# Performance work log

Measured on AMD Instinct MI355X. Metric: run time of the kernel, lower is better.

## Reference

```python
import jax, jax.numpy as jnp
import numpy as np

D_STATE = 512
D_MODEL = 512
BATCH = 8
SEQ = 4096
DT_MIN, DT_MAX = 1e-3, 0.1
LN_EPS = 1e-5


def setup_inputs() -> dict:
    key = jax.random.key(0)
    ks = jax.random.split(key, 4)
    x = jax.random.normal(ks[0], (BATCH, SEQ, D_MODEL), dtype=jnp.float32)
    volatility_scale = jax.random.uniform(ks[1], (BATCH, SEQ, 1), dtype=jnp.float32)
    # parameters (mirroring the torch module's __init__)
    log_lambda_real = jnp.linspace(np.log(DT_MIN), np.log(DT_MAX), D_STATE).astype(jnp.float32)
    log_b = jax.random.uniform(ks[2], (D_STATE, 1), dtype=jnp.float32, minval=-0.5, maxval=0.5)
    c = jax.random.normal(ks[3], (1, D_STATE), dtype=jnp.float32) / np.sqrt(D_STATE)
    log_d = jnp.zeros((1,), jnp.float32)
    ts = np.array([1.0 / 24.0, 1.0, 5.0, 21.0, 63.0], np.float32)
    extra = np.linspace(63.0, 189.0, D_STATE - len(ts), dtype=np.float32)
    log_step = jnp.log(jnp.asarray(np.concatenate([ts, extra])))
    volatility_gate = jnp.ones((D_MODEL,), jnp.float32)
    alpha = jnp.asarray(0.7, jnp.float32)
    ln_weight = jnp.ones((D_STATE,), jnp.float32)
    ln_bias = jnp.zeros((D_STATE,), jnp.float32)
    return dict(x=x, volatility_scale=volatility_scale,
                log_lambda_real=log_lambda_real, log_b=log_b, c=c, log_d=log_d,
                log_step=log_step, volatility_gate=volatility_gate, alpha=alpha,
                ln_weight=ln_weight, ln_bias=ln_bias)


def reference(x, volatility_scale, log_lambda_real, log_b, c, log_d,
              log_step, volatility_gate, alpha, ln_weight, ln_bias):
    lam = -jnp.exp(log_lambda_real)              # [N], negative real poles
    step = jnp.exp(log_step)                     # [N], per-state timescale
    b = jnp.exp(log_b)[:, 0]                     # [N]
    d = jnp.exp(log_d)                           # [1], skip gain
    # bilinear (Tustin) discretization, paired per state
    z = step * lam                               # [N]
    a_disc = (2.0 + z) / (2.0 - z)               # [N]
    b_disc = step * (1.0 + a_disc) * b / 2.0     # [N]
    gate = jax.nn.sigmoid(volatility_gate)       # [D]
    c_vec = c[0]                                 # [N]

    def layer_norm(h):
        mu = jnp.mean(h, axis=-1, keepdims=True)
        var = jnp.var(h, axis=-1, keepdims=True)
        return (h - mu) * jax.lax.rsqrt(var + LN_EPS) * ln_weight + ln_bias

    def scan_step(h, inp):
        x_t, v_t = inp                           # [B,D], [B,1]
        h = a_disc * h + b_disc * x_t            # diagonal SSM update, [B,N]
        h = layer_norm(h)
        h = h / (1.0 + gate * v_t)               # volatility gating
        y_t = jnp.sum(h * c_vec, axis=-1, keepdims=True) + d * x_t  # [B,D]
        return h, y_t

    h0 = jnp.zeros((x.shape[0], a_disc.shape[0]), x.dtype)
    xs = (jnp.swapaxes(x, 0, 1), jnp.swapaxes(volatility_scale, 0, 1))  # time-major
    _, ys = jax.lax.scan(scan_step, h0, xs)      # [S,B,D]
    y = jnp.swapaxes(ys, 0, 1)                   # [B,S,D]
    al = jax.nn.sigmoid(alpha)
    return al * x + (1.0 - al) * y
```

## Files before the change

### kernel.cpp

```cpp
#include <hip/hip_runtime.h>
#include <cstdint>
#include <cstddef>

#define BATCH 8
#define SEQ   4096
#define DS    512
#define JPL   8
#define BLK   8
#define NBLK  (SEQ / BLK)
#define LN_EPS 1e-5f

typedef float v2f __attribute__((ext_vector_type(2)));
typedef float v4f __attribute__((ext_vector_type(4)));

static __device__ __forceinline__ v2f lo2(v4f x) { return __builtin_shufflevector(x, x, 0, 1); }
static __device__ __forceinline__ v2f hi2(v4f x) { return __builtin_shufflevector(x, x, 2, 3); }

template <int CTRL>
__device__ __forceinline__ float dpp_add(float v) {
  int t = __builtin_amdgcn_update_dpp(0, __builtin_bit_cast(int, v), CTRL, 0xF, 0xF, true);
  return v + __builtin_bit_cast(float, t);
}
__device__ __forceinline__ float wave_sum64(float v) {
  v = dpp_add<0x111>(v);
  v = dpp_add<0x112>(v);
  v = dpp_add<0x114>(v);
  v = dpp_add<0x118>(v);
  v = dpp_add<0x142>(v);
  v = dpp_add<0x143>(v);
  return v;
}
__device__ __forceinline__ float bcast63(float v) {
  return __builtin_bit_cast(float, __builtin_amdgcn_readlane(__builtin_bit_cast(int, v), 63));
}

__device__ __forceinline__ void ld16(const float* g, float* l) {
  __builtin_amdgcn_global_load_lds(
      (const __attribute__((address_space(1))) void*)g,
      (__attribute__((address_space(3))) void*)l, 16, 0, 0);
}

__global__ __launch_bounds__(192, 1) void ssm_scan(
    const float* __restrict__ x, const float* __restrict__ vol,
    const float* __restrict__ llr, const float* __restrict__ logb,
    const float* __restrict__ cvec, const float* __restrict__ lstp,
    const float* __restrict__ vgat, const float* __restrict__ lnw,
    const float* __restrict__ lnb, const float* __restrict__ alph,
    const float* __restrict__ logd, float* __restrict__ out)
{
  __shared__ __attribute__((aligned(16))) float X0[4096], X1[4096];
  __shared__ __attribute__((aligned(16))) float R0[4096], R1[4096];
  __shared__ __attribute__((aligned(16))) float SC0[512], SC1[512];
  __shared__ __attribute__((aligned(16))) float SB0[512], SB1[512];

  const int b    = blockIdx.x;
  const int lane = threadIdx.x & 63;
  const int wid  = threadIdx.x >> 6;

  if (wid == 1) {
    const float* xg = x + (size_t)b * SEQ * DS + lane * JPL;
    float* ob = out + (size_t)b * SEQ * DS;
    float al   = 1.0f / (1.0f + expf(-alph[0]));
    float dd   = expf(logd[0]);
    float coef = __builtin_fmaf(1.0f - al, dd, al);
    float c1   = 1.0f - al;

    auto dma_blk = [&](int blk, float* Xs) {
#pragma unroll
      for (int u = 0; u < BLK; ++u) {
        const float* row = xg + (size_t)(blk * BLK + u) * DS;
        ld16(row,     Xs + u * 512);
        ld16(row + 4, Xs + u * 512 + 256);
      }
    };
    auto out_blk = [&](const float* SCs, const float* Xs, int blk) {
#pragma unroll
      for (int u = 0; u < BLK; ++u) {
        float s  = bcast63(wave_sum64(SCs[u * 64 + lane]));
        float sc = c1 * s;
        v4f xa = *(const v4f*)(Xs + u * 512 + lane * 4);
        v4f xb = *(const v4f*)(Xs + u * 512 + 256 + lane * 4);
        v4f ya = xa * coef + sc;
        v4f yb = xb * coef + sc;
        float* row = ob + (size_t)(blk * BLK + u) * DS + lane * 8;
        *(v4f*)(row)     = ya;
        *(v4f*)(row + 4) = yb;
      }
    };

    dma_blk(0, X0);
    __syncthreads();
#pragma unroll 1
    for (int i2 = 0; i2 < NBLK; i2 += 2) {
      if (i2 > 0) {
        out_blk(SC1, X1, i2 - 1);
        asm volatile("s_waitcnt lgkmcnt(0)" ::: "memory");
        __builtin_amdgcn_sched_barrier(0);
      }
      dma_blk(i2 + 1, X1);
      __syncthreads();
      out_blk(SC0, X0, i2);
      if (i2 + 2 < NBLK) {
        asm volatile("s_waitcnt lgkmcnt(0)" ::: "memory");
        __builtin_amdgcn_sched_barrier(0);
        dma_blk(i2 + 2, X0);
      }
      __syncthreads();
    }
    out_blk(SC1, X1, NBLK - 1);
  } else if (wid == 2) {
    v2f gate[4];
#pragma unroll
    for (int j = 0; j < JPL; ++j)
      gate[j >> 1][j & 1] = 1.0f / (1.0f + expf(-vgat[lane * JPL + j]));
    v4f cb0, cb1;
#pragma unroll
    for (int m = 0; m < 4; ++m) {
      int n0 = lane * JPL + m, n1 = lane * JPL + 4 + m;
      cb0[m] = cvec[n0] * lnb[n0];
      cb1[m] = cvec[n1] * lnb[n1];
    }
    const float* vg = vol + (size_t)b * SEQ;

    auto rg_blk = [&](v4f Va, v4f Vb, float* Rs, float* SBs) {
#pragma unroll
      for (int u = 0; u < BLK; ++u) {
        float vt = (u < 4) ? Va[u] : Vb[u - 4];
        v4f r0, r1;
#pragma unroll
        for (int k = 0; k < 4; ++k) {
          v2f den = gate[k] * vt + 1.0f;
          float q0 = __builtin_amdgcn_rcpf(den.x);
          float q1 = __builtin_amdgcn_rcpf(den.y);
          if (k < 2) { r0[2 * k] = q0; r0[2 * k + 1] = q1; }
          else       { r1[2 * (k - 2)] = q0; r1[2 * (k - 2) + 1] = q1; }
        }
        *(v4f*)(Rs + u * 512 + lane * 4)       = r0;
        *(v4f*)(Rs + u * 512 + 256 + lane * 4) = r1;
        v4f md = cb0 * r0;
        md = __builtin_elementwise_fma(cb1, r1, md);
        v2f mh = lo2(md) + hi2(md);
        SBs[u * 64 + lane] = mh.x + mh.y;
      }
    };

    v4f V0a = *(const v4f*)(vg + 0), V0b = *(const v4f*)(vg + 4);
    v4f V1a = *(const v4f*)(vg + 8), V1b = *(const v4f*)(vg + 12);
    rg_blk(V0a, V0b, R0, SB0);
    __syncthreads();
#pragma unroll 1
    for (int i2 = 0; i2 < NBLK; i2 += 2) {
      if (i2 + 2 < NBLK) {
        V0a = *(const v4f*)(vg + (i2 + 2) * BLK);
        V0b = *(const v4f*)(vg + (i2 + 2) * BLK + 4);
      }
      rg_blk(V1a, V1b, R1, SB1);
      __syncthreads();
      if (i2 + 3 < NBLK) {
        V1a = *(const v4f*)(vg + (i2 + 3) * BLK);
        V1b = *(const v4f*)(vg + (i2 + 3) * BLK + 4);
      }
      if (i2 + 2 < NBLK) rg_blk(V0a, V0b, R0, SB0);
      __syncthreads();
    }
  } else {
    v2f bd[4], aw[4], ab[4], cw[4];
#pragma unroll
    for (int j = 0; j < JPL; ++j) {
      int n = lane * JPL + j;
      float lam = -expf(llr[n]);
      float st  = expf(lstp[n]);
      float z   = st * lam;
      float ad  = (2.0f + z) / (2.0f - z);
      float bdv = st * (1.0f + ad) * expf(logb[n]) * 0.5f;
      float wv  = lnw[n], bi = lnb[n], cv = cvec[n];
      bd[j >> 1][j & 1] = bdv;
      aw[j >> 1][j & 1] = ad * wv;
      ab[j >> 1][j & 1] = ad * bi;
      cw[j >> 1][j & 1] = cv * wv;
    }
    v2f hp[4];
#pragma unroll
    for (int k = 0; k < 4; ++k) hp[k] = (v2f){0.0f, 0.0f};

    auto proc_blk = [&](const float* Xs, const float* Rs, const float* SBs, float* SCs) {
#pragma unroll
      for (int u = 0; u < BLK; ++u) {
        v4f xx0 = *(const v4f*)(Xs + u * 512 + lane * 4);
        v4f xx1 = *(const v4f*)(Xs + u * 512 + 256 + lane * 4);
        v4f rr0 = *(const v4f*)(Rs + u * 512 + lane * 4);
        v4f rr1 = *(const v4f*)(Rs + u * 512 + 256 + lane * 4);
        float u3s = SBs[u * 64 + lane];
        v2f xs[4] = {lo2(xx0), hi2(xx0), lo2(xx1), hi2(xx1)};
        v2f rs[4] = {lo2(rr0), hi2(rr0), lo2(rr1), hi2(rr1)};

        v2f hr[4], q[4], abrs[4];
#pragma unroll
        for (int k = 0; k < 4; ++k) {
          hr[k]   = __builtin_elementwise_fma(bd[k], xs[k], hp[k]);
          q[k]    = rs[k] * hr[k];
          abrs[k] = ab[k] * rs[k];
        }
        v2f t01 = hr[0] + hr[1], t23 = hr[2] + hr[3];
        v2f tt  = t01 + t23;
        float s1 = tt.x + tt.y;
        v2f m01 = hr[0] * hr[0];
        m01 = __builtin_elementwise_fma(hr[1], hr[1], m01);
        v2f m23 = hr[2] * hr[2];
        m23 = __builtin_elementwise_fma(hr[3], hr[3], m23);
        v2f mm = m01 + m23;
        float s2 = mm.x + mm.y;

        s1 = bcast63(wave_sum64(s1));
        s2 = bcast63(wave_sum64(s2));
        float mu  = s1 * (1.0f / DS);
        float m2e = __builtin_fmaf(s2, 1.0f / DS, LN_EPS);
        float var = __builtin_fmaf(-mu, mu, m2e);
        float inv = __builtin_amdgcn_rsqf(var);

        v2f muv = {mu, mu}, invv = {inv, inv};
        v2f tv[4];
#pragma unroll
        for (int k = 0; k < 4; ++k)
          tv[k] = __builtin_elementwise_fma(-muv, rs[k], q[k]);
#pragma unroll
        for (int k = 0; k < 4; ++k) {
          v2f sv = aw[k] * tv[k];
          hp[k]  = __builtin_elementwise_fma(invv, sv, abrs[k]);
        }
        v2f u0 = cw[0] * tv[0];
        u0 = __builtin_elementwise_fma(cw[1], tv[1], u0);
        v2f u2 = cw[2] * tv[2];
        u2 = __builtin_elementwise_fma(cw[3], tv[3], u2);
        v2f uu = u0 + u2;
        float u1s = uu.x + uu.y;
        SCs[u * 64 + lane] = __builtin_fmaf(inv, u1s, u3s);
      }
    };

    __syncthreads();
#pragma unroll 1
    for (int i2 = 0; i2 < NBLK; i2 += 2) {
      proc_blk(X0, R0, SB0, SC0);
      __syncthreads();
      proc_blk(X1, R1, SB1, SC1);
      __syncthreads();
    }
  }
}

extern "C" void kernel_launch(void* const* d_in, const int* in_sizes, int n_in,
                              void* d_out, int out_size, void* d_ws, size_t ws_size,
                              hipStream_t stream) {
  const float* x    = (const float*)d_in[0];
  const float* vol  = (const float*)d_in[1];
  const float* llr  = (const float*)d_in[2];
  const float* logb = (const float*)d_in[3];
  const float* cvec = (const float*)d_in[4];
  const float* logd = (const float*)d_in[5];
  const float* lstp = (const float*)d_in[6];
  const float* vgat = (const float*)d_in[7];
  const float* alph = (const float*)d_in[8];
  const float* lnw  = (const float*)d_in[9];
  const float* lnb  = (const float*)d_in[10];
  float* outf = (float*)d_out;

  ssm_scan<<<BATCH, 192, 0, stream>>>(x, vol, llr, logb, cvec, lstp,
                                      vgat, lnw, lnb, alph, logd, outf);
}
```

Baseline: 676.2 us.

## Deepen x prefetch to four LDS buffers with vmcnt-based barriers

The DMA wave now keeps x blocks in a four-slot LDS ring and prefetches two blocks ahead, using explicit vmcnt waits instead of full __syncthreads. All three waves switch to raw s_barrier with lgkmcnt waits, so the barrier no longer drains outstanding global loads. The goal is to hide global-load latency behind the serial scan wave. The cost is more LDS and fragile hand-counted vmcnt thresholds, which could introduce races if the counts are wrong.

```diff
diff --git a/kernel.cpp b/kernel.cpp
--- a/kernel.cpp
+++ b/kernel.cpp
@@ -15,6 +15,9 @@
 
 static __device__ __forceinline__ v2f lo2(v4f x) { return __builtin_shufflevector(x, x, 0, 1); }
 static __device__ __forceinline__ v2f hi2(v4f x) { return __builtin_shufflevector(x, x, 2, 3); }
+
+#define LGKM0() asm volatile("s_waitcnt lgkmcnt(0)" ::: "memory")
+#define BARRIER() __builtin_amdgcn_s_barrier()
 
 template <int CTRL>
 __device__ __forceinline__ float dpp_add(float v) {
@@ -48,7 +51,7 @@
     const float* __restrict__ lnb, const float* __restrict__ alph,
     const float* __restrict__ logd, float* __restrict__ out)
 {
-  __shared__ __attribute__((aligned(16))) float X0[4096], X1[4096];
+  __shared__ __attribute__((aligned(16))) float X[4][4096];
   __shared__ __attribute__((aligned(16))) float R0[4096], R1[4096];
   __shared__ __attribute__((aligned(16))) float SC0[512], SC1[512];
   __shared__ __attribute__((aligned(16))) float SB0[512], SB1[512];
@@ -88,26 +91,27 @@
       }
     };
 
-    dma_blk(0, X0);
-    __syncthreads();
+    dma_blk(0, X[0]);
+    dma_blk(1, X[1]);
+    asm volatile("s_waitcnt vmcnt(16)" ::: "memory");
+    BARRIER();
+    dma_blk(2, X[2]);
+    asm volatile("s_waitcnt vmcnt(16)" ::: "memory");
+    BARRIER();
 #pragma unroll 1
-    for (int i2 = 0; i2 < NBLK; i2 += 2) {
-      if (i2 > 0) {
-        out_blk(SC1, X1, i2 - 1);
-        asm volatile("s_waitcnt lgkmcnt(0)" ::: "memory");
-        __builtin_amdgcn_sched_barrier(0);
-      }
-      dma_blk(i2 + 1, X1);
-      __syncthreads();
-      out_blk(SC0, X0, i2);
-      if (i2 + 2 < NBLK) {
-        asm volatile("s_waitcnt lgkmcnt(0)" ::: "memory");
-        __builtin_amdgcn_sched_barrier(0);
-        dma_blk(i2 + 2, X0);
-      }
-      __syncthreads();
-    }
-    out_blk(SC1, X1, NBLK - 1);
+    for (int j = 1; j < NBLK; ++j) {
+      out_blk((j & 1) ? SC0 : SC1, X[(j - 1) & 3], j - 1);
+      LGKM0();
+      __builtin_amdgcn_sched_barrier(0);
+      if (j + 2 < NBLK) {
+        dma_blk(j + 2, X[(j + 2) & 3]);
+        asm volatile("s_waitcnt vmcnt(32)" ::: "memory");
+      } else if (j + 1 < NBLK) {
+        asm volatile("s_waitcnt vmcnt(16)" ::: "memory");
+      }
+      BARRIER();
+    }
+    out_blk(SC1, X[(NBLK - 1) & 3], NBLK - 1);
   } else if (wid == 2) {
     v2f gate[4];
 #pragma unroll
@@ -147,7 +151,8 @@
     v4f V0a = *(const v4f*)(vg + 0), V0b = *(const v4f*)(vg + 4);
     v4f V1a = *(const v4f*)(vg + 8), V1b = *(const v4f*)(vg + 12);
     rg_blk(V0a, V0b, R0, SB0);
-    __syncthreads();
+    LGKM0();
+    BARRIER();
 #pragma unroll 1
     for (int i2 = 0; i2 < NBLK; i2 += 2) {
       if (i2 + 2 < NBLK) {
@@ -155,13 +160,15 @@
         V0b = *(const v4f*)(vg + (i2 + 2) * BLK + 4);
       }
       rg_blk(V1a, V1b, R1, SB1);
-      __syncthreads();
+      LGKM0();
+      BARRIER();
       if (i2 + 3 < NBLK) {
         V1a = *(const v4f*)(vg + (i2 + 3) * BLK);
         V1b = *(const v4f*)(vg + (i2 + 3) * BLK + 4);
       }
       if (i2 + 2 < NBLK) rg_blk(V0a, V0b, R0, SB0);
-      __syncthreads();
+      LGKM0();
+      BARRIER();
     }
   } else {
     v2f bd[4], aw[4], ab[4], cw[4];
@@ -238,13 +245,13 @@
       }
     };
 
-    __syncthreads();
+    BARRIER();
 #pragma unroll 1
-    for (int i2 = 0; i2 < NBLK; i2 += 2) {
-      proc_blk(X0, R0, SB0, SC0);
-      __syncthreads();
-      proc_blk(X1, R1, SB1, SC1);
-      __syncthreads();
+    for (int i4 = 0; i4 < NBLK; i4 += 4) {
+      proc_blk(X[0], R0, SB0, SC0); LGKM0(); BARRIER();
+      proc_blk(X[1], R1, SB1, SC1); LGKM0(); BARRIER();
+      proc_blk(X[2], R0, SB0, SC0); LGKM0(); BARRIER();
+      proc_blk(X[3], R1, SB1, SC1); LGKM0(); BARRIER();
     }
   }
 }
```

Result: slower. 741.1 us (+9.6%).

## Collapse warp-specialized pipeline into single wave with register double-buffering

Applied to the files above, without the earlier changes.

Replaces the three-wave producer/consumer design (DMA+output wave, gating wave, scan wave communicating via LDS and __syncthreads) with a single 64-thread wave per batch that loads x and volatility into registers two blocks ahead, computes gating inline, and writes output directly. This removes LDS traffic and block barriers from the serial critical path. In exchange the one wave now does all the gating reciprocals, the extra output reduction, and the global stores on the serial chain. It also relies on register prefetch alone to hide global load latency.

```diff
diff --git a/kernel.cpp b/kernel.cpp
--- a/kernel.cpp
+++ b/kernel.cpp
@@ -6,7 +6,7 @@
 #define SEQ   4096
 #define DS    512
 #define JPL   8
-#define BLK   8
+#define BLK   4
 #define NBLK  (SEQ / BLK)
 #define LN_EPS 1e-5f
 
@@ -34,13 +34,7 @@
   return __builtin_bit_cast(float, __builtin_amdgcn_readlane(__builtin_bit_cast(int, v), 63));
 }
 
-__device__ __forceinline__ void ld16(const float* g, float* l) {
-  __builtin_amdgcn_global_load_lds(
-      (const __attribute__((address_space(1))) void*)g,
-      (__attribute__((address_space(3))) void*)l, 16, 0, 0);
-}
-
-__global__ __launch_bounds__(192, 1) void ssm_scan(
+__global__ __launch_bounds__(64, 1) void ssm_scan(
     const float* __restrict__ x, const float* __restrict__ vol,
     const float* __restrict__ llr, const float* __restrict__ logb,
     const float* __restrict__ cvec, const float* __restrict__ lstp,
@@ -48,204 +42,121 @@
     const float* __restrict__ lnb, const float* __restrict__ alph,
     const float* __restrict__ logd, float* __restrict__ out)
 {
-  __shared__ __attribute__((aligned(16))) float X0[4096], X1[4096];
-  __shared__ __attribute__((aligned(16))) float R0[4096], R1[4096];
-  __shared__ __attribute__((aligned(16))) float SC0[512], SC1[512];
-  __shared__ __attribute__((aligned(16))) float SB0[512], SB1[512];
+  const int b    = blockIdx.x;
+  const int lane = threadIdx.x;
 
-  const int b    = blockIdx.x;
-  const int lane = threadIdx.x & 63;
-  const int wid  = threadIdx.x >> 6;
+  v2f bd[4], aw[4], ab[4], cw[4], cb[4], gate[4];
+#pragma unroll
+  for (int j = 0; j < JPL; ++j) {
+    int n = lane * JPL + j;
+    float lam = -expf(llr[n]);
+    float st  = expf(lstp[n]);
+    float z   = st * lam;
+    float ad  = (2.0f + z) / (2.0f - z);
+    float bdv = st * (1.0f + ad) * expf(logb[n]) * 0.5f;
+    float wv  = lnw[n], bi = lnb[n], cv = cvec[n];
+    bd[j >> 1][j & 1]   = bdv;
+    aw[j >> 1][j & 1]   = ad * wv;
+    ab[j >> 1][j & 1]   = ad * bi;
+    gate[j >> 1][j & 1] = 1.0f / (1.0f + expf(-vgat[n]));
+    cw[j >> 1][j & 1]   = cv * wv;
+    cb[j >> 1][j & 1]   = cv * bi;
+  }
+  float al   = 1.0f / (1.0f + expf(-alph[0]));
+  float dd   = expf(logd[0]);
+  float coef = __builtin_fmaf(1.0f - al, dd, al);
+  float c1   = 1.0f - al;
+#pragma unroll
+  for (int k = 0; k < 4; ++k) { cw[k] = cw[k] * c1; cb[k] = cb[k] * c1; }
 
-  if (wid == 1) {
-    const float* xg = x + (size_t)b * SEQ * DS + lane * JPL;
-    float* ob = out + (size_t)b * SEQ * DS;
-    float al   = 1.0f / (1.0f + expf(-alph[0]));
-    float dd   = expf(logd[0]);
-    float coef = __builtin_fmaf(1.0f - al, dd, al);
-    float c1   = 1.0f - al;
+  const float* xg = x   + (size_t)b * SEQ * DS + lane * JPL;
+  float*       og = out + (size_t)b * SEQ * DS + lane * JPL;
+  const float* vg = vol + (size_t)b * SEQ;
 
-    auto dma_blk = [&](int blk, float* Xs) {
+  v2f hp[4];
 #pragma unroll
-      for (int u = 0; u < BLK; ++u) {
-        const float* row = xg + (size_t)(blk * BLK + u) * DS;
-        ld16(row,     Xs + u * 512);
-        ld16(row + 4, Xs + u * 512 + 256);
+  for (int k = 0; k < 4; ++k) hp[k] = (v2f){0.0f, 0.0f};
+
+  v4f XA[BLK][2], XB[BLK][2];
+  v4f VA, VB;
+
+  auto loadblk = [&](int blk, v4f (&X)[BLK][2], v4f& V) {
+    const float* base = xg + (size_t)blk * BLK * DS;
+#pragma unroll
+    for (int u = 0; u < BLK; ++u) {
+      X[u][0] = *(const v4f*)(base + u * DS);
+      X[u][1] = *(const v4f*)(base + u * DS + 4);
+    }
+    V = *(const v4f*)(vg + blk * BLK);
+  };
+
+  auto procblk = [&](int blk, v4f (&X)[BLK][2], v4f& V) {
+    float* ob = og + (size_t)blk * BLK * DS;
+#pragma unroll
+    for (int u = 0; u < BLK; ++u) {
+      float vt = V[u];
+      v2f rs[4];
+#pragma unroll
+      for (int k = 0; k < 4; ++k) {
+        v2f den = gate[k] * vt + 1.0f;
+        rs[k].x = __builtin_amdgcn_rcpf(den.x);
+        rs[k].y = __builtin_amdgcn_rcpf(den.y);
       }
-    };
-    auto out_blk = [&](const float* SCs, const float* Xs, int blk) {
+      v2f xs[4] = {lo2(X[u][0]), hi2(X[u][0]), lo2(X[u][1]), hi2(X[u][1])};
+
+      v2f hr[4];
 #pragma unroll
-      for (int u = 0; u < BLK; ++u) {
-        float s  = bcast63(wave_sum64(SCs[u * 64 + lane]));
-        float sc = c1 * s;
-        v4f xa = *(const v4f*)(Xs + u * 512 + lane * 4);
-        v4f xb = *(const v4f*)(Xs + u * 512 + 256 + lane * 4);
-        v4f ya = xa * coef + sc;
-        v4f yb = xb * coef + sc;
-        float* row = ob + (size_t)(blk * BLK + u) * DS + lane * 8;
-        *(v4f*)(row)     = ya;
-        *(v4f*)(row + 4) = yb;
+      for (int k = 0; k < 4; ++k)
+        hr[k] = __builtin_elementwise_fma(bd[k], xs[k], hp[k]);
+
+      v2f t01 = hr[0] + hr[1], t23 = hr[2] + hr[3];
+      v2f tt  = t01 + t23;
+      float s1 = tt.x + tt.y;
+      v2f m01 = hr[0] * hr[0];
+      m01 = __builtin_elementwise_fma(hr[1], hr[1], m01);
+      v2f m23 = hr[2] * hr[2];
+      m23 = __builtin_elementwise_fma(hr[3], hr[3], m23);
+      v2f mm = m01 + m23;
+      float s2 = mm.x + mm.y;
+
+      s1 = bcast63(wave_sum64(s1));
+      s2 = bcast63(wave_sum64(s2));
+      float mu  = s1 * (1.0f / DS);
+      float m2e = __builtin_fmaf(s2, 1.0f / DS, LN_EPS);
+      float var = __builtin_fmaf(-mu, mu, m2e);
+      float inv = __builtin_amdgcn_rsqf(var);
+
+      v2f muv = {mu, mu}, invv = {inv, inv};
+      v2f u1 = {0.0f, 0.0f}, u3 = {0.0f, 0.0f};
+#pragma unroll
+      for (int k = 0; k < 4; ++k) {
+        v2f hrm  = hr[k] - muv;
+        v2f tv   = rs[k] * hrm;
+        v2f sv   = aw[k] * tv;
+        v2f abrs = ab[k] * rs[k];
+        hp[k] = __builtin_elementwise_fma(invv, sv, abrs);
+        u1 = __builtin_elementwise_fma(cw[k], tv, u1);
+        u3 = __builtin_elementwise_fma(cb[k], rs[k], u3);
       }
-    };
+      v2f dp = __builtin_elementwise_fma(u1, invv, u3);
+      float dl = dp.x + dp.y;
+      float s = bcast63(wave_sum64(dl));
 
-    dma_blk(0, X0);
-    __syncthreads();
+      v4f o0 = X[u][0] * coef + s;
+      v4f o1 = X[u][1] * coef + s;
+      *(v4f*)(ob + (size_t)u * DS)     = o0;
+      *(v4f*)(ob + (size_t)u * DS + 4) = o1;
+    }
+  };
+
+  loadblk(0, XA, VA);
+  loadblk(1, XB, VB);
 #pragma unroll 1
-    for (int i2 = 0; i2 < NBLK; i2 += 2) {
-      if (i2 > 0) {
-        out_blk(SC1, X1, i2 - 1);
-        asm volatile("s_waitcnt lgkmcnt(0)" ::: "memory");
-        __builtin_amdgcn_sched_barrier(0);
-      }
-      dma_blk(i2 + 1, X1);
-      __syncthreads();
-      out_blk(SC0, X0, i2);
-      if (i2 + 2 < NBLK) {
-        asm volatile("s_waitcnt lgkmcnt(0)" ::: "memory");
-        __builtin_amdgcn_sched_barrier(0);
-        dma_blk(i2 + 2, X0);
-      }
-      __syncthreads();
-    }
-    out_blk(SC1, X1, NBLK - 1);
-  } else if (wid == 2) {
-    v2f gate[4];
-#pragma unroll
-    for (int j = 0; j < JPL; ++j)
-      gate[j >> 1][j & 1] = 1.0f / (1.0f + expf(-vgat[lane * JPL + j]));
-    v4f cb0, cb1;
-#pragma unroll
-    for (int m = 0; m < 4; ++m) {
-      int n0 = lane * JPL + m, n1 = lane * JPL + 4 + m;
-      cb0[m] = cvec[n0] * lnb[n0];
-      cb1[m] = cvec[n1] * lnb[n1];
-    }
-    const float* vg = vol + (size_t)b * SEQ;
-
-    auto rg_blk = [&](v4f Va, v4f Vb, float* Rs, float* SBs) {
-#pragma unroll
-      for (int u = 0; u < BLK; ++u) {
-        float vt = (u < 4) ? Va[u] : Vb[u - 4];
-        v4f r0, r1;
-#pragma unroll
-        for (int k = 0; k < 4; ++k) {
-          v2f den = gate[k] * vt + 1.0f;
-          float q0 = __builtin_amdgcn_rcpf(den.x);
-          float q1 = __builtin_amdgcn_rcpf(den.y);
-          if (k < 2) { r0[2 * k] = q0; r0[2 * k + 1] = q1; }
-          else       { r1[2 * (k - 2)] = q0; r1[2 * (k - 2) + 1] = q1; }
-        }
-        *(v4f*)(Rs + u * 512 + lane * 4)       = r0;
-        *(v4f*)(Rs + u * 512 + 256 + lane * 4) = r1;
-        v4f md = cb0 * r0;
-        md = __builtin_elementwise_fma(cb1, r1, md);
-        v2f mh = lo2(md) + hi2(md);
-        SBs[u * 64 + lane] = mh.x + mh.y;
-      }
-    };
-
-    v4f V0a = *(const v4f*)(vg + 0), V0b = *(const v4f*)(vg + 4);
-    v4f V1a = *(const v4f*)(vg + 8), V1b = *(const v4f*)(vg + 12);
-    rg_blk(V0a, V0b, R0, SB0);
-    __syncthreads();
-#pragma unroll 1
-    for (int i2 = 0; i2 < NBLK; i2 += 2) {
-      if (i2 + 2 < NBLK) {
-        V0a = *(const v4f*)(vg + (i2 + 2) * BLK);
-        V0b = *(const v4f*)(vg + (i2 + 2) * BLK + 4);
-      }
-      rg_blk(V1a, V1b, R1, SB1);
-      __syncthreads();
-      if (i2 + 3 < NBLK) {
-        V1a = *(const v4f*)(vg + (i2 + 3) * BLK);
-        V1b = *(const v4f*)(vg + (i2 + 3) * BLK + 4);
-      }
-      if (i2 + 2 < NBLK) rg_blk(V0a, V0b, R0, SB0);
-      __syncthreads();
-    }
-  } else {
-    v2f bd[4], aw[4], ab[4], cw[4];
-#pragma unroll
-    for (int j = 0; j < JPL; ++j) {
-      int n = lane * JPL + j;
-      float lam = -expf(llr[n]);
-      float st  = expf(lstp[n]);
-      float z   = st * lam;
-      float ad  = (2.0f + z) / (2.0f - z);
-      float bdv = st * (1.0f + ad) * expf(logb[n]) * 0.5f;
-      float wv  = lnw[n], bi = lnb[n], cv = cvec[n];
-      bd[j >> 1][j & 1] = bdv;
-      aw[j >> 1][j & 1] = ad * wv;
-      ab[j >> 1][j & 1] = ad * bi;
-      cw[j >> 1][j & 1] = cv * wv;
-    }
-    v2f hp[4];
-#pragma unroll
-    for (int k = 0; k < 4; ++k) hp[k] = (v2f){0.0f, 0.0f};
-
-    auto proc_blk = [&](const float* Xs, const float* Rs, const float* SBs, float* SCs) {
-#pragma unroll
-      for (int u = 0; u < BLK; ++u) {
-        v4f xx0 = *(const v4f*)(Xs + u * 512 + lane * 4);
-        v4f xx1 = *(const v4f*)(Xs + u * 512 + 256 + lane * 4);
-        v4f rr0 = *(const v4f*)(Rs + u * 512 + lane * 4);
-        v4f rr1 = *(const v4f*)(Rs + u * 512 + 256 + lane * 4);
-        float u3s = SBs[u * 64 + lane];
-        v2f xs[4] = {lo2(xx0), hi2(xx0), lo2(xx1), hi2(xx1)};
-        v2f rs[4] = {lo2(rr0), hi2(rr0), lo2(rr1), hi2(rr1)};
-
-        v2f hr[4], q[4], abrs[4];
-#pragma unroll
-        for (int k = 0; k < 4; ++k) {
-          hr[k]   = __builtin_elementwise_fma(bd[k], xs[k], hp[k]);
-          q[k]    = rs[k] * hr[k];
-          abrs[k] = ab[k] * rs[k];
-        }
-        v2f t01 = hr[0] + hr[1], t23 = hr[2] + hr[3];
-        v2f tt  = t01 + t23;
-        float s1 = tt.x + tt.y;
-        v2f m01 = hr[0] * hr[0];
-        m01 = __builtin_elementwise_fma(hr[1], hr[1], m01);
-        v2f m23 = hr[2] * hr[2];
-        m23 = __builtin_elementwise_fma(hr[3], hr[3], m23);
-        v2f mm = m01 + m23;
-        float s2 = mm.x + mm.y;
-
-        s1 = bcast63(wave_sum64(s1));
-        s2 = bcast63(wave_sum64(s2));
-        float mu  = s1 * (1.0f / DS);
-        float m2e = __builtin_fmaf(s2, 1.0f / DS, LN_EPS);
-        float var = __builtin_fmaf(-mu, mu, m2e);
-        float inv = __builtin_amdgcn_rsqf(var);
-
-        v2f muv = {mu, mu}, invv = {inv, inv};
-        v2f tv[4];
-#pragma unroll
-        for (int k = 0; k < 4; ++k)
-          tv[k] = __builtin_elementwise_fma(-muv, rs[k], q[k]);
-#pragma unroll
-        for (int k = 0; k < 4; ++k) {
-          v2f sv = aw[k] * tv[k];
-          hp[k]  = __builtin_elementwise_fma(invv, sv, abrs[k]);
-        }
-        v2f u0 = cw[0] * tv[0];
-        u0 = __builtin_elementwise_fma(cw[1], tv[1], u0);
-        v2f u2 = cw[2] * tv[2];
-        u2 = __builtin_elementwise_fma(cw[3], tv[3], u2);
-        v2f uu = u0 + u2;
-        float u1s = uu.x + uu.y;
-        SCs[u * 64 + lane] = __builtin_fmaf(inv, u1s, u3s);
-      }
-    };
-
-    __syncthreads();
-#pragma unroll 1
-    for (int i2 = 0; i2 < NBLK; i2 += 2) {
-      proc_blk(X0, R0, SB0, SC0);
-      __syncthreads();
-      proc_blk(X1, R1, SB1, SC1);
-      __syncthreads();
-    }
+  for (int k2 = 0; k2 < NBLK; k2 += 2) {
+    procblk(k2, XA, VA);
+    if (k2 + 2 < NBLK) loadblk(k2 + 2, XA, VA);
+    procblk(k2 + 1, XB, VB);
+    if (k2 + 3 < NBLK) loadblk(k2 + 3, XB, VB);
   }
 }
 
@@ -265,6 +176,6 @@
   const float* lnb  = (const float*)d_in[10];
   float* outf = (float*)d_out;
 
-  ssm_scan<<<BATCH, 192, 0, stream>>>(x, vol, llr, logb, cvec, lstp,
-                                      vgat, lnw, lnb, alph, logd, outf);
+  ssm_scan<<<BATCH, 64, 0, stream>>>(x, vol, llr, logb, cvec, lstp,
+                                     vgat, lnw, lnb, alph, logd, outf);
 }
```

New measurement: 1.175 ms. +73.7%, slower.

## Precompute per-step moment partials to remove LayerNorm reductions from the scan critical path

Applied to the files above, without the earlier changes.

The serial scan wave no longer runs two full wave reductions of the post-update state before each LayerNorm. The LayerNorm mean and second moment for the next step are now rebuilt algebraically from scalar moments: per-step partial sums of gate and x-dependent terms, which a helper wave computes ahead of time and another wave reduces into a small table, combined with sums the scan wave takes over its own products. The output-mixing coefficients are also deferred to the output wave. This shortens the dependent chain per timestep, at the cost of triple-buffered shared memory, more cross-wave traffic, and some risk of float cancellation in the expanded variance formula.

```diff
diff --git a/kernel.cpp b/kernel.cpp
--- a/kernel.cpp
+++ b/kernel.cpp
@@ -15,6 +15,8 @@
 
 static __device__ __forceinline__ v2f lo2(v4f x) { return __builtin_shufflevector(x, x, 0, 1); }
 static __device__ __forceinline__ v2f hi2(v4f x) { return __builtin_shufflevector(x, x, 2, 3); }
+
+#define LGKM0() asm volatile("s_waitcnt lgkmcnt(0)" ::: "memory")
 
 template <int CTRL>
 __device__ __forceinline__ float dpp_add(float v) {
@@ -40,6 +42,19 @@
       (__attribute__((address_space(3))) void*)l, 16, 0, 0);
 }
 
+__device__ __forceinline__ float t4s(const v2f* a) {
+  v2f s = (a[0] + a[1]) + (a[2] + a[3]);
+  return s.x + s.y;
+}
+__device__ __forceinline__ float t4m(const v2f* a, const v2f* b) {
+  v2f s = a[0] * b[0];
+  s = __builtin_elementwise_fma(a[1], b[1], s);
+  v2f r = a[2] * b[2];
+  r = __builtin_elementwise_fma(a[3], b[3], r);
+  v2f q = s + r;
+  return q.x + q.y;
+}
+
 __global__ __launch_bounds__(192, 1) void ssm_scan(
     const float* __restrict__ x, const float* __restrict__ vol,
     const float* __restrict__ llr, const float* __restrict__ logb,
@@ -48,10 +63,12 @@
     const float* __restrict__ lnb, const float* __restrict__ alph,
     const float* __restrict__ logd, float* __restrict__ out)
 {
-  __shared__ __attribute__((aligned(16))) float X0[4096], X1[4096];
-  __shared__ __attribute__((aligned(16))) float R0[4096], R1[4096];
-  __shared__ __attribute__((aligned(16))) float SC0[512], SC1[512];
-  __shared__ __attribute__((aligned(16))) float SB0[512], SB1[512];
+  __shared__ __attribute__((aligned(16))) float Xt[3][4096];
+  __shared__ __attribute__((aligned(16))) float RS[3][4096];
+  __shared__ __attribute__((aligned(16))) float PART[2][4096];
+  __shared__ __attribute__((aligned(16))) float RHO[32][8];
+  __shared__ __attribute__((aligned(16))) float AB2[32][2];
+  __shared__ __attribute__((aligned(16))) float SC[2][512];
 
   const int b    = blockIdx.x;
   const int lane = threadIdx.x & 63;
@@ -60,10 +77,10 @@
   if (wid == 1) {
     const float* xg = x + (size_t)b * SEQ * DS + lane * JPL;
     float* ob = out + (size_t)b * SEQ * DS;
-    float al   = 1.0f / (1.0f + expf(-alph[0]));
+    float al_  = 1.0f / (1.0f + expf(-alph[0]));
     float dd   = expf(logd[0]);
-    float coef = __builtin_fmaf(1.0f - al, dd, al);
-    float c1   = 1.0f - al;
+    float coef = __builtin_fmaf(1.0f - al_, dd, al_);
+    float c1   = 1.0f - al_;
 
     auto dma_blk = [&](int blk, float* Xs) {
 #pragma unroll
@@ -73,98 +90,64 @@
         ld16(row + 4, Xs + u * 512 + 256);
       }
     };
-    auto out_blk = [&](const float* SCs, const float* Xs, int blk) {
-#pragma unroll
-      for (int u = 0; u < BLK; ++u) {
-        float s  = bcast63(wave_sum64(SCs[u * 64 + lane]));
-        float sc = c1 * s;
+    auto out_blk = [&](int blk) {
+      const float* Xs  = Xt[blk % 3];
+      const float* SCs = SC[blk & 1];
+#pragma unroll
+      for (int u = 0; u < BLK; ++u) {
+        int s = blk * BLK + u;
+        float msum = bcast63(wave_sum64(SCs[u * 64 + lane]));
+        float a_ = AB2[s & 31][0], b_ = AB2[s & 31][1];
+        float y  = __builtin_fmaf(a_, msum,
+                     __builtin_fmaf(b_, RHO[s & 31][5], RHO[s & 31][6]));
+        float scv = c1 * y;
         v4f xa = *(const v4f*)(Xs + u * 512 + lane * 4);
         v4f xb = *(const v4f*)(Xs + u * 512 + 256 + lane * 4);
-        v4f ya = xa * coef + sc;
-        v4f yb = xb * coef + sc;
-        float* row = ob + (size_t)(blk * BLK + u) * DS + lane * 8;
-        *(v4f*)(row)     = ya;
-        *(v4f*)(row + 4) = yb;
-      }
-    };
-
-    dma_blk(0, X0);
+        float* row = ob + (size_t)s * DS + lane * 8;
+        *(v4f*)(row)     = xa * coef + scv;
+        *(v4f*)(row + 4) = xb * coef + scv;
+      }
+    };
+    auto reduce_part = [&](int blk) {
+      const float* P = PART[blk & 1];
+#pragma unroll
+      for (int u = 0; u < BLK; ++u) {
+        v4f pA = *(const v4f*)(P + u * 512 + lane * 8);
+        v4f pB = *(const v4f*)(P + u * 512 + lane * 8 + 4);
+        float r0 = bcast63(wave_sum64(pA[0]));
+        float r1 = bcast63(wave_sum64(pA[1]));
+        float r2 = bcast63(wave_sum64(pA[2]));
+        float r3 = bcast63(wave_sum64(pA[3]));
+        float r4 = bcast63(wave_sum64(pB[0]));
+        float r5 = bcast63(wave_sum64(pB[1]));
+        float r6 = bcast63(wave_sum64(pB[2]));
+        if (lane == 0) {
+          int s = (blk * BLK + u) & 31;
+          RHO[s][0] = r0; RHO[s][1] = r1; RHO[s][2] = r2; RHO[s][3] = r3;
+          RHO[s][4] = r4; RHO[s][5] = r5; RHO[s][6] = r6;
+        }
+      }
+    };
+
+    dma_blk(0, Xt[0]);
+    __syncthreads();
+    reduce_part(0);
+    LGKM0();
+    __builtin_amdgcn_sched_barrier(0);
+    dma_blk(1, Xt[1]);
     __syncthreads();
 #pragma unroll 1
-    for (int i2 = 0; i2 < NBLK; i2 += 2) {
-      if (i2 > 0) {
-        out_blk(SC1, X1, i2 - 1);
-        asm volatile("s_waitcnt lgkmcnt(0)" ::: "memory");
-        __builtin_amdgcn_sched_barrier(0);
-      }
-      dma_blk(i2 + 1, X1);
+    for (int i = 0; i < NBLK; ++i) {
+      if (i >= 1) out_blk(i - 1);
+      LGKM0();
+      __builtin_amdgcn_sched_barrier(0);
+      if (i + 2 < NBLK) dma_blk(i + 2, Xt[(i + 2) % 3]);
+      if (i + 1 < NBLK) reduce_part(i + 1);
       __syncthreads();
-      out_blk(SC0, X0, i2);
-      if (i2 + 2 < NBLK) {
-        asm volatile("s_waitcnt lgkmcnt(0)" ::: "memory");
-        __builtin_amdgcn_sched_barrier(0);
-        dma_blk(i2 + 2, X0);
-      }
-      __syncthreads();
-    }
-    out_blk(SC1, X1, NBLK - 1);
+    }
+    out_blk(NBLK - 1);
   } else if (wid == 2) {
-    v2f gate[4];
-#pragma unroll
-    for (int j = 0; j < JPL; ++j)
-      gate[j >> 1][j & 1] = 1.0f / (1.0f + expf(-vgat[lane * JPL + j]));
-    v4f cb0, cb1;
-#pragma unroll
-    for (int m = 0; m < 4; ++m) {
-      int n0 = lane * JPL + m, n1 = lane * JPL + 4 + m;
-      cb0[m] = cvec[n0] * lnb[n0];
-      cb1[m] = cvec[n1] * lnb[n1];
-    }
-    const float* vg = vol + (size_t)b * SEQ;
-
-    auto rg_blk = [&](v4f Va, v4f Vb, float* Rs, float* SBs) {
-#pragma unroll
-      for (int u = 0; u < BLK; ++u) {
-        float vt = (u < 4) ? Va[u] : Vb[u - 4];
-        v4f r0, r1;
-#pragma unroll
-        for (int k = 0; k < 4; ++k) {
-          v2f den = gate[k] * vt + 1.0f;
-          float q0 = __builtin_amdgcn_rcpf(den.x);
-          float q1 = __builtin_amdgcn_rcpf(den.y);
-          if (k < 2) { r0[2 * k] = q0; r0[2 * k + 1] = q1; }
-          else       { r1[2 * (k - 2)] = q0; r1[2 * (k - 2) + 1] = q1; }
-        }
-        *(v4f*)(Rs + u * 512 + lane * 4)       = r0;
-        *(v4f*)(Rs + u * 512 + 256 + lane * 4) = r1;
-        v4f md = cb0 * r0;
-        md = __builtin_elementwise_fma(cb1, r1, md);
-        v2f mh = lo2(md) + hi2(md);
-        SBs[u * 64 + lane] = mh.x + mh.y;
-      }
-    };
-
-    v4f V0a = *(const v4f*)(vg + 0), V0b = *(const v4f*)(vg + 4);
-    v4f V1a = *(const v4f*)(vg + 8), V1b = *(const v4f*)(vg + 12);
-    rg_blk(V0a, V0b, R0, SB0);
-    __syncthreads();
-#pragma unroll 1
-    for (int i2 = 0; i2 < NBLK; i2 += 2) {
-      if (i2 + 2 < NBLK) {
-        V0a = *(const v4f*)(vg + (i2 + 2) * BLK);
-        V0b = *(const v4f*)(vg + (i2 + 2) * BLK + 4);
-      }
-      rg_blk(V1a, V1b, R1, SB1);
-      __syncthreads();
-      if (i2 + 3 < NBLK) {
-        V1a = *(const v4f*)(vg + (i2 + 3) * BLK);
-        V1b = *(const v4f*)(vg + (i2 + 3) * BLK + 4);
-      }
-      if (i2 + 2 < NBLK) rg_blk(V0a, V0b, R0, SB0);
-      __syncthreads();
-    }
-  } else {
-    v2f bd[4], aw[4], ab[4], cw[4];
+    v2f gate[4], awc[4], abc[4], cwc[4], cbc[4], bdv[4];
 #pragma unroll
     for (int j = 0; j < JPL; ++j) {
       int n = lane * JPL + j;
@@ -172,78 +155,177 @@
       float st  = expf(lstp[n]);
       float z   = st * lam;
       float ad  = (2.0f + z) / (2.0f - z);
-      float bdv = st * (1.0f + ad) * expf(logb[n]) * 0.5f;
+      float bdd = st * (1.0f + ad) * expf(logb[n]) * 0.5f;
       float wv  = lnw[n], bi = lnb[n], cv = cvec[n];
-      bd[j >> 1][j & 1] = bdv;
-      aw[j >> 1][j & 1] = ad * wv;
-      ab[j >> 1][j & 1] = ad * bi;
-      cw[j >> 1][j & 1] = cv * wv;
-    }
-    v2f hp[4];
-#pragma unroll
-    for (int k = 0; k < 4; ++k) hp[k] = (v2f){0.0f, 0.0f};
-
-    auto proc_blk = [&](const float* Xs, const float* Rs, const float* SBs, float* SCs) {
-#pragma unroll
-      for (int u = 0; u < BLK; ++u) {
-        v4f xx0 = *(const v4f*)(Xs + u * 512 + lane * 4);
-        v4f xx1 = *(const v4f*)(Xs + u * 512 + 256 + lane * 4);
-        v4f rr0 = *(const v4f*)(Rs + u * 512 + lane * 4);
-        v4f rr1 = *(const v4f*)(Rs + u * 512 + 256 + lane * 4);
-        float u3s = SBs[u * 64 + lane];
-        v2f xs[4] = {lo2(xx0), hi2(xx0), lo2(xx1), hi2(xx1)};
-        v2f rs[4] = {lo2(rr0), hi2(rr0), lo2(rr1), hi2(rr1)};
-
-        v2f hr[4], q[4], abrs[4];
+      gate[j >> 1][j & 1] = 1.0f / (1.0f + expf(-vgat[n]));
+      awc[j >> 1][j & 1]  = ad * wv;
+      abc[j >> 1][j & 1]  = ad * bi;
+      cwc[j >> 1][j & 1]  = cv * wv;
+      cbc[j >> 1][j & 1]  = cv * bi;
+      bdv[j >> 1][j & 1]  = bdd;
+    }
+    const float* xq = x + (size_t)b * SEQ * DS + lane * JPL;
+    const float* vg = vol + (size_t)b * SEQ;
+
+    v4f XP[16];
+    v4f VPa, VPb;
+
+    auto pf = [&](int blk) {
+      VPa = *(const v4f*)(vg + blk * BLK);
+      VPb = *(const v4f*)(vg + blk * BLK + 4);
+#pragma unroll
+      for (int u = 0; u < BLK; ++u) {
+        int r = blk * BLK + u + 1;
+        if (r > SEQ - 1) r = SEQ - 1;
+        XP[2 * u]     = *(const v4f*)(xq + (size_t)r * DS);
+        XP[2 * u + 1] = *(const v4f*)(xq + (size_t)r * DS + 4);
+      }
+    };
+    auto work = [&](int blk) {
+      float* RSs = RS[blk % 3];
+      float* Pp  = PART[blk & 1];
+#pragma unroll
+      for (int u = 0; u < BLK; ++u) {
+        float vt = (u < 4) ? VPa[u] : VPb[u - 4];
+        v2f rsv[4];
 #pragma unroll
         for (int k = 0; k < 4; ++k) {
-          hr[k]   = __builtin_elementwise_fma(bd[k], xs[k], hp[k]);
-          q[k]    = rs[k] * hr[k];
-          abrs[k] = ab[k] * rs[k];
+          v2f den = gate[k] * vt + 1.0f;
+          rsv[k].x = __builtin_amdgcn_rcpf(den.x);
+          rsv[k].y = __builtin_amdgcn_rcpf(den.y);
         }
-        v2f t01 = hr[0] + hr[1], t23 = hr[2] + hr[3];
-        v2f tt  = t01 + t23;
-        float s1 = tt.x + tt.y;
-        v2f m01 = hr[0] * hr[0];
-        m01 = __builtin_elementwise_fma(hr[1], hr[1], m01);
-        v2f m23 = hr[2] * hr[2];
-        m23 = __builtin_elementwise_fma(hr[3], hr[3], m23);
-        v2f mm = m01 + m23;
-        float s2 = mm.x + mm.y;
-
-        s1 = bcast63(wave_sum64(s1));
-        s2 = bcast63(wave_sum64(s2));
-        float mu  = s1 * (1.0f / DS);
-        float m2e = __builtin_fmaf(s2, 1.0f / DS, LN_EPS);
-        float var = __builtin_fmaf(-mu, mu, m2e);
-        float inv = __builtin_amdgcn_rsqf(var);
-
-        v2f muv = {mu, mu}, invv = {inv, inv};
-        v2f tv[4];
-#pragma unroll
-        for (int k = 0; k < 4; ++k)
-          tv[k] = __builtin_elementwise_fma(-muv, rs[k], q[k]);
+        v4f r03 = {rsv[0].x, rsv[0].y, rsv[1].x, rsv[1].y};
+        v4f r47 = {rsv[2].x, rsv[2].y, rsv[3].x, rsv[3].y};
+        *(v4f*)(RSs + u * 512 + lane * 4)       = r03;
+        *(v4f*)(RSs + u * 512 + 256 + lane * 4) = r47;
+        v2f xr[4] = {lo2(XP[2 * u]), hi2(XP[2 * u]),
+                     lo2(XP[2 * u + 1]), hi2(XP[2 * u + 1])};
+        v2f Qv[4], Rv[4], cwv[4], cbv[4];
 #pragma unroll
         for (int k = 0; k < 4; ++k) {
-          v2f sv = aw[k] * tv[k];
-          hp[k]  = __builtin_elementwise_fma(invv, sv, abrs[k]);
+          Qv[k]  = awc[k] * rsv[k];
+          Rv[k]  = __builtin_elementwise_fma(bdv[k], xr[k], abc[k] * rsv[k]);
+          cwv[k] = cwc[k] * rsv[k];
+          cbv[k] = cbc[k] * rsv[k];
         }
-        v2f u0 = cw[0] * tv[0];
-        u0 = __builtin_elementwise_fma(cw[1], tv[1], u0);
-        v2f u2 = cw[2] * tv[2];
-        u2 = __builtin_elementwise_fma(cw[3], tv[3], u2);
-        v2f uu = u0 + u2;
-        float u1s = uu.x + uu.y;
-        SCs[u * 64 + lane] = __builtin_fmaf(inv, u1s, u3s);
-      }
-    };
-
+        float pQ  = t4s(Qv),  pQQ = t4m(Qv, Qv), pQR = t4m(Qv, Rv);
+        float pR  = t4s(Rv),  pRR = t4m(Rv, Rv);
+        float pcw = t4s(cwv), pcb = t4s(cbv);
+        *(v4f*)(Pp + u * 512 + lane * 8)     = (v4f){pQ, pQQ, pQR, pR};
+        *(v4f*)(Pp + u * 512 + lane * 8 + 4) = (v4f){pRR, pcw, pcb, 0.0f};
+      }
+    };
+
+    pf(0); work(0);
+    __syncthreads();
+    pf(1); work(1);
+    if (2 < NBLK) pf(2);
     __syncthreads();
 #pragma unroll 1
-    for (int i2 = 0; i2 < NBLK; i2 += 2) {
-      proc_blk(X0, R0, SB0, SC0);
+    for (int i = 0; i < NBLK; ++i) {
+      if (i + 2 < NBLK) work(i + 2);
+      if (i + 3 < NBLK) pf(i + 3);
       __syncthreads();
-      proc_blk(X1, R1, SB1, SC1);
+    }
+  } else {
+    v2f aw[4], abc2[4], cwc2[4], bdv[4];
+#pragma unroll
+    for (int j = 0; j < JPL; ++j) {
+      int n = lane * JPL + j;
+      float lam = -expf(llr[n]);
+      float st  = expf(lstp[n]);
+      float z   = st * lam;
+      float ad  = (2.0f + z) / (2.0f - z);
+      float bdd = st * (1.0f + ad) * expf(logb[n]) * 0.5f;
+      float wv  = lnw[n], bi = lnb[n], cv = cvec[n];
+      aw[j >> 1][j & 1]   = ad * wv;
+      abc2[j >> 1][j & 1] = ad * bi;
+      cwc2[j >> 1][j & 1] = cv * wv;
+      bdv[j >> 1][j & 1]  = bdd;
+    }
+    v2f hr[4];
+    float al = 0.0f, be = 0.0f;
+    float sU = 0.0f, sUU = 0.0f, sUQ = 0.0f, sUR = 0.0f;
+
+    auto cstep = [&](int t, const float* RSs, const float* xrow, bool first0) {
+      const int u = t & 7;
+      const int s = (t - 1) & 31;
+      v4f rs0 = *(const v4f*)(RSs + u * 512 + lane * 4);
+      v4f rs1 = *(const v4f*)(RSs + u * 512 + 256 + lane * 4);
+      v4f xa  = *(const v4f*)(xrow + lane * 4);
+      v4f xb  = *(const v4f*)(xrow + 256 + lane * 4);
+      float S1h, S2h;
+      if (first0) {
+        float s1 = t4s(hr);
+        float s2 = t4m(hr, hr);
+        S1h = bcast63(wave_sum64(s1));
+        S2h = bcast63(wave_sum64(s2));
+      } else {
+        v4f rhoA = *(const v4f*)(&RHO[s][0]);
+        float rhoRR = RHO[s][4];
+        float t0 = __builtin_fmaf(be, rhoA[0], rhoA[3]);
+        S1h = __builtin_fmaf(al, sU, t0);
+        float a2 = al * al, tw = al + al;
+        float ab2 = tw * be, b2 = be * be, bb = be + be;
+        float X3 = __builtin_fmaf(bb, rhoA[2], rhoRR);
+        X3 = __builtin_fmaf(b2, rhoA[1], X3);
+        X3 = __builtin_fmaf(tw, sUR, X3);
+        X3 = __builtin_fmaf(ab2, sUQ, X3);
+        S2h = __builtin_fmaf(a2, sUU, X3);
+      }
+      float mu  = S1h * (1.0f / DS);
+      float m2e = __builtin_fmaf(S2h, 1.0f / DS, LN_EPS);
+      float var = __builtin_fmaf(-mu, mu, m2e);
+      float inv = __builtin_amdgcn_rsqf(var);
+      al = inv;
+      be = -inv * mu;
+      if (lane == 0) { AB2[t & 31][0] = al; AB2[t & 31][1] = be; }
+      v2f rsv[4] = {lo2(rs0), hi2(rs0), lo2(rs1), hi2(rs1)};
+      v2f xs[4]  = {lo2(xa), hi2(xa), lo2(xb), hi2(xb)};
+      v2f Qv[4], Rv[4], uv[4], mv[4];
+#pragma unroll
+      for (int k = 0; k < 4; ++k) {
+        Qv[k] = aw[k] * rsv[k];
+        Rv[k] = __builtin_elementwise_fma(bdv[k], xs[k], abc2[k] * rsv[k]);
+        uv[k] = Qv[k] * hr[k];
+        mv[k] = (cwc2[k] * rsv[k]) * hr[k];
+      }
+      float su  = t4s(uv);
+      float suu = t4m(uv, uv);
+      float suq = t4m(uv, Qv);
+      float sur = t4m(uv, Rv);
+      float sm  = t4s(mv);
+      SC[(t >> 3) & 1][u * 64 + lane] = sm;
+      v2f av = {al, al}, bv = {be, be};
+#pragma unroll
+      for (int k = 0; k < 4; ++k)
+        hr[k] = __builtin_elementwise_fma(av, uv[k],
+                  __builtin_elementwise_fma(bv, Qv[k], Rv[k]));
+      sU  = bcast63(wave_sum64(su));
+      sUU = bcast63(wave_sum64(suu));
+      sUQ = bcast63(wave_sum64(suq));
+      sUR = bcast63(wave_sum64(sur));
+    };
+
+    __syncthreads();
+    __syncthreads();
+    {
+      v4f x0a = *(const v4f*)(Xt[0] + lane * 4);
+      v4f x0b = *(const v4f*)(Xt[0] + 256 + lane * 4);
+      v2f xs0[4] = {lo2(x0a), hi2(x0a), lo2(x0b), hi2(x0b)};
+#pragma unroll
+      for (int k = 0; k < 4; ++k) hr[k] = bdv[k] * xs0[k];
+    }
+#pragma unroll 1
+    for (int i = 0; i < NBLK; ++i) {
+      const float* RSs = RS[i % 3];
+      const float* Xc  = Xt[i % 3];
+      const float* Xn  = Xt[(i + 1) % 3];
+#pragma unroll
+      for (int u = 0; u < BLK; ++u) {
+        const float* xrow = (u < 7) ? (Xc + (u + 1) * 512) : Xn;
+        cstep(i * BLK + u, RSs, xrow, (u == 0) && (i == 0));
+      }
       __syncthreads();
     }
   }
```

New measurement: 1.866 ms. 176% more time.
